# Kernel optimization log

Measured on AMD Instinct MI355X. Metric: run time of the kernel, lower is better.

The kernel has to match this reference:

```python
import jax, jax.numpy as jnp
import numpy as np

H, C = 8, 32          # heads, per-head channels (h_feats)
NEG_SLOPE = 0.2


def setup_inputs() -> dict:
    key = jax.random.key(0)
    ks = jax.random.split(key, 9)
    N, E, F_IN, F_E = 50000, 800000, 128, 16
    x = jax.random.normal(ks[0], (N, F_IN), jnp.float32)
    edge_index = jax.random.randint(ks[1], (2, E), 0, N, jnp.int64)
    edge_attr = jax.random.normal(ks[2], (E, F_E), jnp.float32)
    s = 1.0 / np.sqrt(F_IN)
    W = jax.random.normal(ks[3], (H * C, F_IN), jnp.float32) * s
    W_edge = jax.random.normal(ks[4], (H * C, F_E), jnp.float32) * (1.0 / np.sqrt(F_E))
    att_src = jax.random.normal(ks[5], (H, C), jnp.float32) * (1.0 / np.sqrt(C))
    att_dst = jax.random.normal(ks[6], (H, C), jnp.float32) * (1.0 / np.sqrt(C))
    att_edge = jax.random.normal(ks[7], (H, C), jnp.float32) * (1.0 / np.sqrt(C))
    bias = jnp.zeros((C,), jnp.float32)
    return {"x": x, "edge_index": edge_index, "edge_attr": edge_attr,
            "W": W, "W_edge": W_edge, "att_src": att_src, "att_dst": att_dst,
            "att_edge": att_edge, "bias": bias}


def reference(x, edge_index, edge_attr, W, W_edge, att_src, att_dst, att_edge, bias):
    N = x.shape[0]
    src, dst = edge_index[0], edge_index[1]

    # --- add self loops, edge_attr fill_value='mean' (per-dst mean of incoming attrs) ---
    deg = jax.ops.segment_sum(jnp.ones_like(dst, dtype=edge_attr.dtype), dst, num_segments=N)
    loop_attr = jax.ops.segment_sum(edge_attr, dst, num_segments=N) / jnp.maximum(deg, 1.0)[:, None]
    loop = jnp.arange(N, dtype=src.dtype)
    src = jnp.concatenate([src, loop])
    dst = jnp.concatenate([dst, loop])
    ea = jnp.concatenate([edge_attr, loop_attr], axis=0)  # [E+N, F_e]

    # --- node projection and per-node attention terms ---
    xh = (x @ W.T).reshape(N, H, C)                      # [N,H,C]
    a_src = jnp.einsum('nhc,hc->nh', xh, att_src)        # [N,H]
    a_dst = jnp.einsum('nhc,hc->nh', xh, att_dst)        # [N,H]

    # edge attention folded: (lin_edge(e).view(E,H,C) * att_edge).sum(-1) == e @ M
    M = jnp.einsum('hcf,hc->fh', W_edge.reshape(H, C, -1), att_edge)  # [F_e,H]
    a_edge = ea @ M                                      # [E+N,H]

    alpha = a_src[src] + a_dst[dst] + a_edge             # [E+N,H]
    alpha = jnp.where(alpha >= 0, alpha, NEG_SLOPE * alpha)

    # --- scatter-softmax over edges grouped by dst node ---
    amax = jax.ops.segment_max(alpha, dst, num_segments=N)  # every node has a self loop
    ex = jnp.exp(alpha - amax[dst])
    denom = jax.ops.segment_sum(ex, dst, num_segments=N)
    att = ex / denom[dst]                                # [E+N,H]

    # --- weighted message scatter-sum ---
    msg = xh[src] * att[..., None]                       # [E+N,H,C]
    out = jax.ops.segment_sum(msg, dst, num_segments=N)  # [N,H,C]
    return out.mean(axis=1) + bias                       # concat=False -> head mean
```

## Files before the change

kernel.cpp:

```cpp
#include <hip/hip_runtime.h>
#include <math.h>

#define H 8
#define C 32
#define HC 256
#define FE 16
#define FIN 128
#define NEG_SLOPE 0.2f

typedef __attribute__((ext_vector_type(8))) short bf16x8;
typedef __attribute__((ext_vector_type(4))) float f32x4;

__device__ __forceinline__ unsigned short f2bf(float f) {
  unsigned int u = __float_as_uint(f);
  unsigned int lsb = (u >> 16) & 1u;
  u += 0x7fffu + lsb;
  return (unsigned short)(u >> 16);
}
__device__ __forceinline__ float bf2f(unsigned short s) {
  return __uint_as_float(((unsigned int)s) << 16);
}

__device__ __forceinline__ void split8(const float* v, bf16x8& hi, bf16x8& lo) {
#pragma unroll
  for (int i = 0; i < 8; ++i) {
    unsigned int u = __float_as_uint(v[i]);
    unsigned int hu = u & 0xffff0000u;
    float r = v[i] - __uint_as_float(hu);
    hi[i] = (short)(hu >> 16);
    lo[i] = (short)f2bf(r);
  }
}

__global__ __launch_bounds__(256) void k_xh(const float* __restrict__ x,
                                            const unsigned short* __restrict__ Whi,
                                            const unsigned short* __restrict__ Wlo,
                                            const float* __restrict__ att_src,
                                            const float* __restrict__ att_dst,
                                            unsigned short* __restrict__ xhb,
                                            float* __restrict__ a_src,
                                            float* __restrict__ a_dst, int N) {
  int t = threadIdx.x;
  int w = t >> 6, lane = t & 63;
  int n15 = lane & 15, q = lane >> 4;
  int nodeBase = blockIdx.x * 128 + w * 32;
  int chBase = blockIdx.y * 128;

  f32x4 acc[8][2];
#pragma unroll
  for (int mt = 0; mt < 8; ++mt)
#pragma unroll
    for (int nt = 0; nt < 2; ++nt) acc[mt][nt] = (f32x4)(0.f);

  for (int ks = 0; ks < 4; ++ks) {
    int kOff = ks * 32 + q * 8;
    bf16x8 Bhi[2], Blo[2];
#pragma unroll
    for (int nt = 0; nt < 2; ++nt) {
      int node = nodeBase + nt * 16 + n15;
      int rn = (node < N) ? node : (N - 1);
      const float* px = &x[(size_t)rn * FIN + kOff];
      float vb[8];
      *(float4*)&vb[0] = *(const float4*)px;
      *(float4*)&vb[4] = *(const float4*)(px + 4);
      split8(vb, Bhi[nt], Blo[nt]);
    }
#pragma unroll
    for (int mt = 0; mt < 8; ++mt) {
      int widx = ((chBase + mt * 16 + n15) << 7) + kOff;
      bf16x8 Ahi = *(const bf16x8*)&Whi[widx];
      bf16x8 Alo = *(const bf16x8*)&Wlo[widx];
#pragma unroll
      for (int nt = 0; nt < 2; ++nt) {
        acc[mt][nt] = __builtin_amdgcn_mfma_f32_16x16x32_bf16(Ahi, Bhi[nt], acc[mt][nt], 0, 0, 0);
        acc[mt][nt] = __builtin_amdgcn_mfma_f32_16x16x32_bf16(Ahi, Blo[nt], acc[mt][nt], 0, 0, 0);
        acc[mt][nt] = __builtin_amdgcn_mfma_f32_16x16x32_bf16(Alo, Bhi[nt], acc[mt][nt], 0, 0, 0);
      }
    }
  }

  float ps[2][4] = {{0.f,0.f,0.f,0.f},{0.f,0.f,0.f,0.f}};
  float pd[2][4] = {{0.f,0.f,0.f,0.f},{0.f,0.f,0.f,0.f}};
#pragma unroll
  for (int mt = 0; mt < 8; ++mt) {
    int hl = mt >> 1;
#pragma unroll
    for (int r = 0; r < 4; ++r) {
      int ch = chBase + mt * 16 + q * 4 + r;
      float as_c = att_src[ch], ad_c = att_dst[ch];
#pragma unroll
      for (int nt = 0; nt < 2; ++nt) {
        float val = acc[mt][nt][r];
        ps[nt][hl] = fmaf(val, as_c, ps[nt][hl]);
        pd[nt][hl] = fmaf(val, ad_c, pd[nt][hl]);
      }
    }
#pragma unroll
    for (int nt = 0; nt < 2; ++nt) {
      int node = nodeBase + nt * 16 + n15;
      if (node < N) {
        ushort4 us;
        us.x = f2bf(acc[mt][nt][0]); us.y = f2bf(acc[mt][nt][1]);
        us.z = f2bf(acc[mt][nt][2]); us.w = f2bf(acc[mt][nt][3]);
        *(ushort4*)&xhb[(size_t)node * HC + chBase + mt * 16 + q * 4] = us;
      }
    }
  }
#pragma unroll
  for (int nt = 0; nt < 2; ++nt)
#pragma unroll
    for (int hl = 0; hl < 4; ++hl) {
      ps[nt][hl] += __shfl_xor(ps[nt][hl], 16, 64);
      ps[nt][hl] += __shfl_xor(ps[nt][hl], 32, 64);
      pd[nt][hl] += __shfl_xor(pd[nt][hl], 16, 64);
      pd[nt][hl] += __shfl_xor(pd[nt][hl], 32, 64);
    }
  if (q == 0) {
#pragma unroll
    for (int nt = 0; nt < 2; ++nt) {
      int node = nodeBase + nt * 16 + n15;
      if (node < N) {
        *(float4*)&a_src[node * H + blockIdx.y * 4] = make_float4(ps[nt][0], ps[nt][1], ps[nt][2], ps[nt][3]);
        *(float4*)&a_dst[node * H + blockIdx.y * 4] = make_float4(pd[nt][0], pd[nt][1], pd[nt][2], pd[nt][3]);
      }
    }
  }
}

__global__ __launch_bounds__(256) void k_deg(const int* __restrict__ ei,
                                             int* __restrict__ deg,
                                             int* __restrict__ rank,
                                             const float* __restrict__ W,
                                             unsigned short* __restrict__ Whi,
                                             unsigned short* __restrict__ Wlo, int E) {
  int e = blockIdx.x * 256 + threadIdx.x;
  if (e < HC * FIN) {
    float v = W[e];
    unsigned int u = __float_as_uint(v);
    unsigned int hu = u & 0xffff0000u;
    Whi[e] = (unsigned short)(hu >> 16);
    Wlo[e] = f2bf(v - __uint_as_float(hu));
  }
  if (e < E) rank[e] = atomicAdd(&deg[ei[E + e]], 1);
}

__global__ __launch_bounds__(256) void k_scan1(const int* __restrict__ deg,
                                               int* __restrict__ bsum, int N) {
  int t = threadIdx.x;
  int i = blockIdx.x * 256 + t;
  int v = (i < N) ? deg[i] : 0;
#pragma unroll
  for (int m = 1; m < 64; m <<= 1) v += __shfl_xor(v, m, 64);
  __shared__ int wsum[4];
  if ((t & 63) == 0) wsum[t >> 6] = v;
  __syncthreads();
  if (t == 0) bsum[blockIdx.x] = wsum[0] + wsum[1] + wsum[2] + wsum[3];
}

__global__ __launch_bounds__(256) void k_scan23(const int* __restrict__ deg,
                                                const int* __restrict__ bsum,
                                                int* __restrict__ rowptr, int N, int E, int nb) {
  __shared__ int sb[256];
  __shared__ int buf[256];
  int t = threadIdx.x;
  sb[t] = (t < nb) ? bsum[t] : 0;
  int i = blockIdx.x * 256 + t;
  int v = (i < N) ? deg[i] : 0;
  buf[t] = v;
  __syncthreads();
  for (int off = 1; off < 256; off <<= 1) {
    int y1 = (t >= off) ? sb[t - off] : 0;
    int y2 = (t >= off) ? buf[t - off] : 0;
    __syncthreads();
    sb[t] += y1;
    buf[t] += y2;
    __syncthreads();
  }
  int bofs = (blockIdx.x == 0) ? 0 : sb[blockIdx.x - 1];
  if (i < N) rowptr[i] = bofs + buf[t] - v;
  if (i == 0) rowptr[N] = E;
}

__global__ __launch_bounds__(256) void k_edge_scatter(const int* __restrict__ ei,
                                                      const float* __restrict__ ea,
                                                      const float* __restrict__ W_edge,
                                                      const float* __restrict__ att_edge,
                                                      const int* __restrict__ rowptr,
                                                      const int* __restrict__ rank,
                                                      unsigned short* __restrict__ recs, int E) {
  __shared__ float Ms[FE * H];
  int t = threadIdx.x;
  if (t < FE * H) {
    int f = t >> 3, h = t & 7;
    float acc = 0.f;
#pragma unroll
    for (int c = 0; c < C; ++c)
      acc += W_edge[(h * C + c) * FE + f] * att_edge[h * C + c];
    Ms[f * H + h] = acc;
  }
  __syncthreads();
  int e = blockIdx.x * 256 + t;
  if (e >= E) return;
  int s = ei[e], d = ei[E + e];
  const float4* p = (const float4*)&ea[(size_t)e * FE];
  float4 v0 = p[0], v1 = p[1], v2 = p[2], v3 = p[3];
  float eav[FE] = {v0.x, v0.y, v0.z, v0.w, v1.x, v1.y, v1.z, v1.w,
                   v2.x, v2.y, v2.z, v2.w, v3.x, v3.y, v3.z, v3.w};
  float o[H];
#pragma unroll
  for (int h = 0; h < H; ++h) {
    float acc = 0.f;
#pragma unroll
    for (int f = 0; f < FE; ++f) acc += eav[f] * Ms[f * H + h];
    o[h] = acc;
  }
  int pos = rowptr[d] + rank[e];
  uint4 pk;
  pk.x = (unsigned int)f2bf(o[0]) | ((unsigned int)f2bf(o[1]) << 16);
  pk.y = (unsigned int)f2bf(o[2]) | ((unsigned int)f2bf(o[3]) << 16);
  pk.z = (unsigned int)f2bf(o[4]) | ((unsigned int)f2bf(o[5]) << 16);
  pk.w = (unsigned int)f2bf(o[6]) | ((unsigned int)f2bf(o[7]) << 16);
  uint4 hv; hv.x = (unsigned int)s; hv.y = 0; hv.z = 0; hv.w = 0;
  unsigned short* rp = &recs[(size_t)pos * 16];
  *(uint4*)rp = pk;
  *(uint4*)(rp + 8) = hv;
}

__global__ __launch_bounds__(256) void k_node(const unsigned short* __restrict__ xhb,
                                              const float* __restrict__ a_src,
                                              const float* __restrict__ a_dst,
                                              const unsigned short* __restrict__ recs,
                                              const int* __restrict__ rowptr,
                                              const float* __restrict__ bias,
                                              float* __restrict__ out, int N) {
  __shared__ float wlds[4][512];
  __shared__ int   slds[4][64];
  int wv = threadIdx.x >> 6;
  int lane = threadIdx.x & 63;
  int n = blockIdx.x * 4 + wv;
  if (n >= N) return;
  int start = rowptr[n];
  int deg = rowptr[n + 1] - start;
  int jmax = (deg < 64) ? deg : 64;
  int padded = (jmax + 7) & ~7;
  int h = lane & 7, esub = lane >> 3;
  float adst = a_dst[n * H + h];
  float asrc = a_src[n * H + h];

  float ae[8]; int sr[8];
#pragma unroll
  for (int it = 0; it < 8; ++it) {
    int j = it * 8 + esub;
    ae[it] = 0.f; sr[it] = 0;
    if (j < jmax) {
      const unsigned short* rp = &recs[(size_t)(start + j) * 16];
      ae[it] = bf2f(rp[h]);
      sr[it] = *(const int*)(rp + 8);
    }
  }
  float asg[8];
#pragma unroll
  for (int it = 0; it < 8; ++it) {
    int j = it * 8 + esub;
    asg[it] = (j < jmax) ? a_src[sr[it] * H + h] : 0.f;
  }
  if (h == 0) {
#pragma unroll
    for (int it = 0; it < 8; ++it) {
      int j = it * 8 + esub;
      if (j < jmax) slds[wv][j] = sr[it];
    }
  }
  {
    int pj = jmax + esub;
    if (pj < padded) {
      if (h == 0) slds[wv][pj] = n;
      wlds[wv][pj * 8 + h] = 0.f;
    }
  }
  float al[8];
  float pmax = -1e30f, psum = 0.f;
#pragma unroll
  for (int it = 0; it < 8; ++it) {
    int j = it * 8 + esub;
    float a = -1e30f;
    if (j < jmax) {
      psum += ae[it];
      a = asg[it] + adst + ae[it];
      a = (a >= 0.f) ? a : NEG_SLOPE * a;
      pmax = fmaxf(pmax, a);
    }
    al[it] = a;
  }
  for (int j0 = 64; j0 < deg; j0 += 8) {
    int j = j0 + esub;
    if (j < deg) {
      const unsigned short* rp = &recs[(size_t)(start + j) * 16];
      float aev = bf2f(rp[h]);
      int src = *(const int*)(rp + 8);
      psum += aev;
      float a = a_src[src * H + h] + adst + aev;
      a = (a >= 0.f) ? a : NEG_SLOPE * a;
      pmax = fmaxf(pmax, a);
    }
  }
#pragma unroll
  for (int m = 8; m <= 32; m <<= 1) {
    pmax = fmaxf(pmax, __shfl_xor(pmax, m, 64));
    psum += __shfl_xor(psum, m, 64);
  }
  float aself = asrc + adst + psum / fmaxf((float)deg, 1.f);
  aself = (aself >= 0.f) ? aself : NEG_SLOPE * aself;
  float amax = fmaxf(pmax, aself);

  float den = 0.f;
#pragma unroll
  for (int it = 0; it < 8; ++it) {
    int j = it * 8 + esub;
    if (j < jmax) {
      float wj = __expf(al[it] - amax);
      den += wj;
      wlds[wv][j * 8 + h] = wj;
    }
  }
  for (int j0 = 64; j0 < deg; j0 += 8) {
    int j = j0 + esub;
    if (j < deg) {
      const unsigned short* rp = &recs[(size_t)(start + j) * 16];
      float aev = bf2f(rp[h]);
      int src = *(const int*)(rp + 8);
      float a = a_src[src * H + h] + adst + aev;
      a = (a >= 0.f) ? a : NEG_SLOPE * a;
      den += __expf(a - amax);
    }
  }
#pragma unroll
  for (int m = 8; m <= 32; m <<= 1) den += __shfl_xor(den, m, 64);
  float wself = __expf(aself - amax);
  float inv = 1.f / (den + wself);

  int hc = lane >> 3;
  float inv_c  = __shfl(inv, hc, 64);
  float ws_c   = __shfl(wself, hc, 64);
  float amax_c = __shfl(amax, hc, 64);
  float adst_c = __shfl(adst, hc, 64);
  float accx, accy, accz, accw;
  {
    uint2 u = ((const uint2*)(xhb + (((size_t)n) << 8)))[lane];
    accx = ws_c * __uint_as_float(u.x << 16);
    accy = ws_c * __uint_as_float(u.x & 0xffff0000u);
    accz = ws_c * __uint_as_float(u.y << 16);
    accw = ws_c * __uint_as_float(u.y & 0xffff0000u);
  }
  for (int j0 = 0; j0 < padded; j0 += 8) {
    uint2 v[8]; float wj[8];
#pragma unroll
    for (int k = 0; k < 8; ++k) {
      wj[k] = wlds[wv][(j0 + k) * 8 + hc];
      v[k] = ((const uint2*)(xhb + (((size_t)slds[wv][j0 + k]) << 8)))[lane];
    }
#pragma unroll
    for (int k = 0; k < 8; ++k) {
      accx = fmaf(__uint_as_float(v[k].x << 16), wj[k], accx);
      accy = fmaf(__uint_as_float(v[k].x & 0xffff0000u), wj[k], accy);
      accz = fmaf(__uint_as_float(v[k].y << 16), wj[k], accz);
      accw = fmaf(__uint_as_float(v[k].y & 0xffff0000u), wj[k], accw);
    }
  }
  for (int j = 64; j < deg; ++j) {
    const unsigned short* rp = &recs[(size_t)(start + j) * 16];
    float aev = bf2f(rp[hc]);
    int src = *(const int*)(rp + 8);
    float a = a_src[src * H + hc] + adst_c + aev;
    a = (a >= 0.f) ? a : NEG_SLOPE * a;
    float wj = __expf(a - amax_c);
    uint2 v = ((const uint2*)(xhb + (((size_t)src) << 8)))[lane];
    accx = fmaf(__uint_as_float(v.x << 16), wj, accx);
    accy = fmaf(__uint_as_float(v.x & 0xffff0000u), wj, accy);
    accz = fmaf(__uint_as_float(v.y << 16), wj, accz);
    accw = fmaf(__uint_as_float(v.y & 0xffff0000u), wj, accw);
  }
  accx *= inv_c; accy *= inv_c; accz *= inv_c; accw *= inv_c;

#pragma unroll
  for (int m = 8; m <= 32; m <<= 1) {
    accx += __shfl_xor(accx, m, 64);
    accy += __shfl_xor(accy, m, 64);
    accz += __shfl_xor(accz, m, 64);
    accw += __shfl_xor(accw, m, 64);
  }
  if (lane < 8) {
    float4 b = ((const float4*)bias)[lane];
    float4 o;
    o.x = accx * 0.125f + b.x;
    o.y = accy * 0.125f + b.y;
    o.z = accz * 0.125f + b.z;
    o.w = accw * 0.125f + b.w;
    ((float4*)&out[(size_t)n * C])[lane] = o;
  }
}

extern "C" void kernel_launch(void* const* d_in, const int* in_sizes, int n_in,
                              void* d_out, int out_size, void* d_ws, size_t ws_size,
                              hipStream_t stream) {
  const float* x        = (const float*)d_in[0];
  const int*   ei       = (const int*)d_in[1];
  const float* ea       = (const float*)d_in[2];
  const float* W        = (const float*)d_in[3];
  const float* W_edge   = (const float*)d_in[4];
  const float* att_src  = (const float*)d_in[5];
  const float* att_dst  = (const float*)d_in[6];
  const float* att_edge = (const float*)d_in[7];
  const float* bias     = (const float*)d_in[8];
  float* out = (float*)d_out;

  int N = in_sizes[0] / FIN;
  int E = in_sizes[1] / 2;
  int nb = (N + 255) / 256;

  char* ws = (char*)d_ws;
  auto take = [&](size_t bytes) {
    char* p = ws;
    ws += (bytes + 255) & ~(size_t)255;
    return p;
  };
  unsigned short* xhb    = (unsigned short*)take((size_t)N * HC * 2);
  float*          a_src  = (float*)take((size_t)N * H * 4);
  float*          a_dst  = (float*)take((size_t)N * H * 4);
  unsigned short* recs   = (unsigned short*)take((size_t)E * 32);
  unsigned short* Whi    = (unsigned short*)take((size_t)HC * FIN * 2);
  unsigned short* Wlo    = (unsigned short*)take((size_t)HC * FIN * 2);
  int*            deg    = (int*)take((size_t)N * 4);
  int*            rowptr = (int*)take((size_t)(N + 1) * 4);
  int*            rank   = (int*)take((size_t)E * 4);
  int*            bsum   = (int*)take((size_t)nb * 4);

  hipMemsetAsync(deg, 0, (size_t)N * 4, stream);
  k_deg<<<(E + 255) / 256, 256, 0, stream>>>(ei, deg, rank, W, Whi, Wlo, E);
  k_xh<<<dim3((N + 127) / 128, 2), 256, 0, stream>>>(x, Whi, Wlo, att_src, att_dst, xhb, a_src, a_dst, N);
  k_scan1<<<nb, 256, 0, stream>>>(deg, bsum, N);
  k_scan23<<<nb, 256, 0, stream>>>(deg, bsum, rowptr, N, E, nb);
  k_edge_scatter<<<(E + 255) / 256, 256, 0, stream>>>(ei, ea, W_edge, att_edge, rowptr, rank, recs, E);
  k_node<<<(N + 3) / 4, 256, 0, stream>>>(xhb, a_src, a_dst, recs, rowptr, bias, out, N);
}
```

Baseline: 302.7 us.

## Precompute a_src into fp16 edge records and split source indices into separate array

The edge-scatter kernel now gathers a_src[src] per edge and stores, for each head, a packed fp16 pair (a_edge + a_src, a_edge) alongside a separate source-index array. This moves the random a_src gather out of the per-node kernel, where it sat on the softmax critical path, into the edge kernel. The node kernel then reads the records coalesced, using lane-contiguous loads. The price is an extra random gather in the edge kernel and fp16 instead of bf16 precision for the attention logits.

```diff
diff --git a/kernel.cpp b/kernel.cpp
--- a/kernel.cpp
+++ b/kernel.cpp
@@ -1,4 +1,5 @@
 #include <hip/hip_runtime.h>
+#include <hip/hip_fp16.h>
 #include <math.h>
 
 #define H 8
@@ -19,6 +20,12 @@
 }
 __device__ __forceinline__ float bf2f(unsigned short s) {
   return __uint_as_float(((unsigned int)s) << 16);
+}
+__device__ __forceinline__ unsigned short f2h(float f) {
+  return __half_as_ushort(__float2half(f));
+}
+__device__ __forceinline__ float h2f(unsigned short s) {
+  return __half2float(__ushort_as_half(s));
 }
 
 __device__ __forceinline__ void split8(const float* v, bf16x8& hi, bf16x8& lo) {
@@ -185,9 +192,11 @@
                                                       const float* __restrict__ ea,
                                                       const float* __restrict__ W_edge,
                                                       const float* __restrict__ att_edge,
+                                                      const float* __restrict__ a_src,
                                                       const int* __restrict__ rowptr,
                                                       const int* __restrict__ rank,
-                                                      unsigned short* __restrict__ recs, int E) {
+                                                      unsigned int* __restrict__ recs,
+                                                      int* __restrict__ sarr, int E) {
   __shared__ float Ms[FE * H];
   int t = threadIdx.x;
   if (t < FE * H) {
@@ -214,22 +223,25 @@
     for (int f = 0; f < FE; ++f) acc += eav[f] * Ms[f * H + h];
     o[h] = acc;
   }
+  const float4* pa = (const float4*)&a_src[(size_t)s * H];
+  float4 a0 = pa[0], a1 = pa[1];
+  float asv[H] = {a0.x, a0.y, a0.z, a0.w, a1.x, a1.y, a1.z, a1.w};
   int pos = rowptr[d] + rank[e];
-  uint4 pk;
-  pk.x = (unsigned int)f2bf(o[0]) | ((unsigned int)f2bf(o[1]) << 16);
-  pk.y = (unsigned int)f2bf(o[2]) | ((unsigned int)f2bf(o[3]) << 16);
-  pk.z = (unsigned int)f2bf(o[4]) | ((unsigned int)f2bf(o[5]) << 16);
-  pk.w = (unsigned int)f2bf(o[6]) | ((unsigned int)f2bf(o[7]) << 16);
-  uint4 hv; hv.x = (unsigned int)s; hv.y = 0; hv.z = 0; hv.w = 0;
-  unsigned short* rp = &recs[(size_t)pos * 16];
-  *(uint4*)rp = pk;
-  *(uint4*)(rp + 8) = hv;
+  unsigned int rec[H];
+#pragma unroll
+  for (int h = 0; h < H; ++h)
+    rec[h] = (unsigned int)f2h(o[h] + asv[h]) | ((unsigned int)f2h(o[h]) << 16);
+  uint4* rp = (uint4*)&recs[(size_t)pos * 8];
+  rp[0] = make_uint4(rec[0], rec[1], rec[2], rec[3]);
+  rp[1] = make_uint4(rec[4], rec[5], rec[6], rec[7]);
+  sarr[pos] = s;
 }
 
 __global__ __launch_bounds__(256) void k_node(const unsigned short* __restrict__ xhb,
                                               const float* __restrict__ a_src,
                                               const float* __restrict__ a_dst,
-                                              const unsigned short* __restrict__ recs,
+                                              const unsigned int* __restrict__ recs,
+                                              const int* __restrict__ sarr,
                                               const int* __restrict__ rowptr,
                                               const float* __restrict__ bias,
                                               float* __restrict__ out, int N) {
@@ -242,65 +254,37 @@
   int start = rowptr[n];
   int deg = rowptr[n + 1] - start;
   int jmax = (deg < 64) ? deg : 64;
-  int padded = (jmax + 7) & ~7;
+  int nit = (jmax + 7) >> 3;
+  int padded = nit << 3;
   int h = lane & 7, esub = lane >> 3;
   float adst = a_dst[n * H + h];
   float asrc = a_src[n * H + h];
 
-  float ae[8]; int sr[8];
-#pragma unroll
-  for (int it = 0; it < 8; ++it) {
-    int j = it * 8 + esub;
-    ae[it] = 0.f; sr[it] = 0;
-    if (j < jmax) {
-      const unsigned short* rp = &recs[(size_t)(start + j) * 16];
-      ae[it] = bf2f(rp[h]);
-      sr[it] = *(const int*)(rp + 8);
-    }
-  }
-  float asg[8];
-#pragma unroll
-  for (int it = 0; it < 8; ++it) {
-    int j = it * 8 + esub;
-    asg[it] = (j < jmax) ? a_src[sr[it] * H + h] : 0.f;
-  }
-  if (h == 0) {
-#pragma unroll
-    for (int it = 0; it < 8; ++it) {
-      int j = it * 8 + esub;
-      if (j < jmax) slds[wv][j] = sr[it];
-    }
-  }
-  {
-    int pj = jmax + esub;
-    if (pj < padded) {
-      if (h == 0) slds[wv][pj] = n;
-      wlds[wv][pj * 8 + h] = 0.f;
-    }
-  }
+  if (lane < padded) slds[wv][lane] = (lane < jmax) ? sarr[start + lane] : n;
+
+  const unsigned int* rb = recs + (size_t)start * 8 + lane;
   float al[8];
   float pmax = -1e30f, psum = 0.f;
 #pragma unroll
   for (int it = 0; it < 8; ++it) {
-    int j = it * 8 + esub;
-    float a = -1e30f;
-    if (j < jmax) {
-      psum += ae[it];
-      a = asg[it] + adst + ae[it];
-      a = (a >= 0.f) ? a : NEG_SLOPE * a;
-      pmax = fmaxf(pmax, a);
-    }
-    al[it] = a;
+    al[it] = -1e30f;
+    if (it < nit) {
+      int j = it * 8 + esub;
+      unsigned int u = (j < jmax) ? rb[it * 64] : 0u;
+      psum += h2f((unsigned short)(u >> 16));
+      float a = h2f((unsigned short)(u & 0xffffu)) + adst;
+      a = fmaxf(a, NEG_SLOPE * a);
+      al[it] = (j < jmax) ? a : -1e30f;
+      pmax = fmaxf(pmax, al[it]);
+    }
   }
   for (int j0 = 64; j0 < deg; j0 += 8) {
     int j = j0 + esub;
     if (j < deg) {
-      const unsigned short* rp = &recs[(size_t)(start + j) * 16];
-      float aev = bf2f(rp[h]);
-      int src = *(const int*)(rp + 8);
-      psum += aev;
-      float a = a_src[src * H + h] + adst + aev;
-      a = (a >= 0.f) ? a : NEG_SLOPE * a;
+      unsigned int u = recs[(size_t)(start + j) * 8 + h];
+      psum += h2f((unsigned short)(u >> 16));
+      float a = h2f((unsigned short)(u & 0xffffu)) + adst;
+      a = fmaxf(a, NEG_SLOPE * a);
       pmax = fmaxf(pmax, a);
     }
   }
@@ -310,27 +294,23 @@
     psum += __shfl_xor(psum, m, 64);
   }
   float aself = asrc + adst + psum / fmaxf((float)deg, 1.f);
-  aself = (aself >= 0.f) ? aself : NEG_SLOPE * aself;
+  aself = fmaxf(aself, NEG_SLOPE * aself);
   float amax = fmaxf(pmax, aself);
 
   float den = 0.f;
 #pragma unroll
-  for (int it = 0; it < 8; ++it) {
-    int j = it * 8 + esub;
-    if (j < jmax) {
+  for (int it = 0; it < 8; ++it)
+    if (it < nit) {
       float wj = __expf(al[it] - amax);
       den += wj;
-      wlds[wv][j * 8 + h] = wj;
-    }
-  }
+      wlds[wv][it * 64 + lane] = wj;
+    }
   for (int j0 = 64; j0 < deg; j0 += 8) {
     int j = j0 + esub;
     if (j < deg) {
-      const unsigned short* rp = &recs[(size_t)(start + j) * 16];
-      float aev = bf2f(rp[h]);
-      int src = *(const int*)(rp + 8);
-      float a = a_src[src * H + h] + adst + aev;
-      a = (a >= 0.f) ? a : NEG_SLOPE * a;
+      unsigned int u = recs[(size_t)(start + j) * 8 + h];
+      float a = h2f((unsigned short)(u & 0xffffu)) + adst;
+      a = fmaxf(a, NEG_SLOPE * a);
       den += __expf(a - amax);
     }
   }
@@ -368,11 +348,10 @@
     }
   }
   for (int j = 64; j < deg; ++j) {
-    const unsigned short* rp = &recs[(size_t)(start + j) * 16];
-    float aev = bf2f(rp[hc]);
-    int src = *(const int*)(rp + 8);
-    float a = a_src[src * H + hc] + adst_c + aev;
-    a = (a >= 0.f) ? a : NEG_SLOPE * a;
+    unsigned int u = recs[(size_t)(start + j) * 8 + hc];
+    int src = sarr[start + j];
+    float a = h2f((unsigned short)(u & 0xffffu)) + adst_c;
+    a = fmaxf(a, NEG_SLOPE * a);
     float wj = __expf(a - amax_c);
     uint2 v = ((const uint2*)(xhb + (((size_t)src) << 8)))[lane];
     accx = fmaf(__uint_as_float(v.x << 16), wj, accx);
@@ -427,7 +406,8 @@
   unsigned short* xhb    = (unsigned short*)take((size_t)N * HC * 2);
   float*          a_src  = (float*)take((size_t)N * H * 4);
   float*          a_dst  = (float*)take((size_t)N * H * 4);
-  unsigned short* recs   = (unsigned short*)take((size_t)E * 32);
+  unsigned int*   recs   = (unsigned int*)take((size_t)E * 32);
+  int*            sarr   = (int*)take((size_t)E * 4);
   unsigned short* Whi    = (unsigned short*)take((size_t)HC * FIN * 2);
   unsigned short* Wlo    = (unsigned short*)take((size_t)HC * FIN * 2);
   int*            deg    = (int*)take((size_t)N * 4);
@@ -440,6 +420,6 @@
   k_xh<<<dim3((N + 127) / 128, 2), 256, 0, stream>>>(x, Whi, Wlo, att_src, att_dst, xhb, a_src, a_dst, N);
   k_scan1<<<nb, 256, 0, stream>>>(deg, bsum, N);
   k_scan23<<<nb, 256, 0, stream>>>(deg, bsum, rowptr, N, E, nb);
-  k_edge_scatter<<<(E + 255) / 256, 256, 0, stream>>>(ei, ea, W_edge, att_edge, rowptr, rank, recs, E);
-  k_node<<<(N + 3) / 4, 256, 0, stream>>>(xhb, a_src, a_dst, recs, rowptr, bias, out, N);
-}
+  k_edge_scatter<<<(E + 255) / 256, 256, 0, stream>>>(ei, ea, W_edge, att_edge, a_src, rowptr, rank, recs, sarr, E);
+  k_node<<<(N + 3) / 4, 256, 0, stream>>>(xhb, a_src, a_dst, recs, sarr, rowptr, bias, out, N);
+}
```

After: 312.3 us. +3.2%, slower.
